# Optimization experiments

Measured on AMD Instinct MI355X. Metric: run time of the kernel, lower is better.

The kernel has to match this reference:

```python
import jax, jax.numpy as jnp
import numpy as np

N_QUBITS = 4
DIM = 2 ** N_QUBITS  # 16
B = 524288


def apply_1q(state, mat, wire):
    """Apply a 2x2 gate (mat: [2,2] or batched [B,2,2]) to `wire` of state [B,16]."""
    b = state.shape[0]
    s = state.reshape((b,) + (2,) * N_QUBITS)
    s = jnp.moveaxis(s, wire + 1, -1)
    shp = s.shape
    s = s.reshape(b, -1, 2)
    if mat.ndim == 3:
        s = jnp.einsum('bij,bkj->bki', mat, s)
    else:
        s = jnp.einsum('ij,bkj->bki', mat, s)
    s = jnp.moveaxis(s.reshape(shp), -1, wire + 1)
    return s.reshape(b, DIM)


def apply_2q(state, mat4, w1, w2):
    """Apply a 4x4 gate to wires (w1, w2) of state [B,16]; w1 is the high bit."""
    b = state.shape[0]
    s = state.reshape((b,) + (2,) * N_QUBITS)
    s = jnp.moveaxis(s, (w1 + 1, w2 + 1), (-2, -1))
    shp = s.shape
    s = s.reshape(b, -1, 4)
    s = jnp.einsum('ij,bkj->bki', mat4, s)
    s = jnp.moveaxis(s.reshape(shp), (-2, -1), (w1 + 1, w2 + 1))
    return s.reshape(b, DIM)


def rx_mat(t):
    c = jnp.cos(t / 2).astype(jnp.complex64)
    s = jnp.sin(t / 2).astype(jnp.complex64)
    return jnp.stack([jnp.stack([c, -1j * s]), jnp.stack([-1j * s, c])])


def ry_mat(t):
    c = jnp.cos(t / 2).astype(jnp.complex64)
    s = jnp.sin(t / 2).astype(jnp.complex64)
    return jnp.stack([jnp.stack([c, -s]), jnp.stack([s, c])])


def rz_mat(t):
    e0 = jnp.exp(-0.5j * t.astype(jnp.complex64))
    e1 = jnp.exp(0.5j * t.astype(jnp.complex64))
    z = jnp.zeros_like(e0)
    return jnp.stack([jnp.stack([e0, z]), jnp.stack([z, e1])])


CNOT = jnp.array([[1, 0, 0, 0],
                  [0, 1, 0, 0],
                  [0, 0, 0, 1],
                  [0, 0, 1, 0]], dtype=jnp.complex64)

# PauliZ sign table: sign of bit i (wire 0 = most significant axis) for each basis index
_idx = np.arange(DIM)
Z_SIGNS = jnp.asarray(
    1.0 - 2.0 * ((_idx[None, :] >> (N_QUBITS - 1 - np.arange(N_QUBITS)[:, None])) & 1),
    dtype=jnp.float32)  # [n_qubits, 16]


def setup_inputs() -> dict:
    key = jax.random.key(0)
    k1, k2 = jax.random.split(key)
    x = jax.random.normal(k1, (B, N_QUBITS), dtype=jnp.float32)
    params = jax.random.normal(k2, (6,), dtype=jnp.float32)
    return {"x": x, "params": params}


def reference(x, params):
    b = x.shape[0]
    state = jnp.zeros((b, DIM), jnp.complex64).at[:, 0].set(1.0)

    # --- RY encoding: angle x[:, i] on wire i (batched 2x2 matrices) ---
    for i in range(N_QUBITS):
        th = x[:, i]
        c = jnp.cos(th / 2).astype(jnp.complex64)
        s = jnp.sin(th / 2).astype(jnp.complex64)
        row0 = jnp.stack([c, -s], axis=-1)
        row1 = jnp.stack([s, c], axis=-1)
        mat = jnp.stack([row0, row1], axis=-2)  # [B,2,2]
        state = apply_1q(state, mat, i)

    # --- RandomLayer: fixed deterministic structure of 8 ops (6 rotations + 2 CNOTs) ---
    state = apply_1q(state, rx_mat(params[0]), 0)
    state = apply_1q(state, ry_mat(params[1]), 1)
    state = apply_1q(state, rz_mat(params[2]), 2)
    state = apply_1q(state, rx_mat(params[3]), 3)
    state = apply_2q(state, CNOT, 0, 1)
    state = apply_2q(state, CNOT, 2, 3)
    state = apply_1q(state, ry_mat(params[4]), 2)
    state = apply_1q(state, rz_mat(params[5]), 0)

    # --- MeasureAll(PauliZ): <Z_i> = sum_k |amp_k|^2 * sign(bit_i(k)) ---
    probs = state.real ** 2 + state.imag ** 2  # [B,16]
    return probs @ Z_SIGNS.T  # [B, n_qubits]
```

## Files before the change

kernel.cpp:

```cpp
#include <hip/hip_runtime.h>

struct cplx { float re, im; };

__device__ __forceinline__ cplx cmul(cplx a, cplx b) {
    return { a.re * b.re - a.im * b.im, a.re * b.im + a.im * b.re };
}
__device__ __forceinline__ cplx cadd(cplx a, cplx b) { return { a.re + b.re, a.im + b.im }; }

template<int MASK>
__device__ __forceinline__ void apply1(cplx st[16], cplx m00, cplx m01, cplx m10, cplx m11) {
#pragma unroll
    for (int i = 0; i < 16; ++i) {
        if (i & MASK) continue;
        cplx a0 = st[i], a1 = st[i | MASK];
        st[i]        = cadd(cmul(m00, a0), cmul(m01, a1));
        st[i | MASK] = cadd(cmul(m10, a0), cmul(m11, a1));
    }
}

__device__ __forceinline__ void cswap(cplx& a, cplx& b) { cplx t = a; a = b; b = t; }

__global__ __launch_bounds__(256) void qfilter_kernel(const float4* __restrict__ x,
                                                      const float* __restrict__ params,
                                                      float4* __restrict__ out, int B) {
    int b = blockIdx.x * blockDim.x + threadIdx.x;
    if (b >= B) return;

    float4 xv = x[b];
    float cx[4], sx[4];
    sincosf(0.5f * xv.x, &sx[0], &cx[0]);
    sincosf(0.5f * xv.y, &sx[1], &cx[1]);
    sincosf(0.5f * xv.z, &sx[2], &cx[2]);
    sincosf(0.5f * xv.w, &sx[3], &cx[3]);

    cplx st[16];
#pragma unroll
    for (int i = 0; i < 16; ++i) {
        float a = (((i >> 3) & 1) ? sx[0] : cx[0]) *
                  (((i >> 2) & 1) ? sx[1] : cx[1]) *
                  (((i >> 1) & 1) ? sx[2] : cx[2]) *
                  (((i     ) & 1) ? sx[3] : cx[3]);
        st[i] = { a, 0.0f };
    }

    float p0 = params[0], p1 = params[1], p2 = params[2], p3 = params[3], p4 = params[4];
    float c, s;

    sincosf(0.5f * p0, &s, &c);
    apply1<8>(st, {c, 0.f}, {0.f, -s}, {0.f, -s}, {c, 0.f});

    sincosf(0.5f * p1, &s, &c);
    apply1<4>(st, {c, 0.f}, {-s, 0.f}, {s, 0.f}, {c, 0.f});

    sincosf(0.5f * p2, &s, &c);
    apply1<2>(st, {c, -s}, {0.f, 0.f}, {0.f, 0.f}, {c, s});

    sincosf(0.5f * p3, &s, &c);
    apply1<1>(st, {c, 0.f}, {0.f, -s}, {0.f, -s}, {c, 0.f});

    cswap(st[8], st[12]); cswap(st[9], st[13]); cswap(st[10], st[14]); cswap(st[11], st[15]);

    cswap(st[2], st[3]); cswap(st[6], st[7]); cswap(st[10], st[11]); cswap(st[14], st[15]);

    sincosf(0.5f * p4, &s, &c);
    apply1<2>(st, {c, 0.f}, {-s, 0.f}, {s, 0.f}, {c, 0.f});


    float e0 = 0.f, e1 = 0.f, e2 = 0.f, e3 = 0.f;
#pragma unroll
    for (int i = 0; i < 16; ++i) {
        float pr = st[i].re * st[i].re + st[i].im * st[i].im;
        e0 += ((i >> 3) & 1) ? -pr : pr;
        e1 += ((i >> 2) & 1) ? -pr : pr;
        e2 += ((i >> 1) & 1) ? -pr : pr;
        e3 += ((i     ) & 1) ? -pr : pr;
    }
    out[b] = make_float4(e0, e1, e2, e3);
}

extern "C" void kernel_launch(void* const* d_in, const int* in_sizes, int n_in,
                              void* d_out, int out_size, void* d_ws, size_t ws_size,
                              hipStream_t stream) {
    const int B = in_sizes[0] / 4;
    const float4* x      = (const float4*)d_in[0];
    const float*  params = (const float*)d_in[1];
    float4*       out    = (float4*)d_out;

    const int threads = 256;
    const int blocks = (B + threads - 1) / threads;
    qfilter_kernel<<<blocks, threads, 0, stream>>>(x, params, out, B);
}
```

Before: 73.80 us.

## Replace statevector simulation with closed-form Pauli-Z expectation formulas

Derives analytic expressions for each qubit's <Z> expectation from the fixed circuit structure. This replaces the 16-amplitude complex statevector evolution with a few cosine and sine evaluations and products per sample. It also switches to fast intrinsics (__cosf/__sincosf), which trades accuracy for speed, and the derivation has to match the reference circuit exactly. The kernel is likely memory-bound, so the gain may come mostly from dropping instructions and registers.

```diff
diff --git a/kernel.cpp b/kernel.cpp
--- a/kernel.cpp
+++ b/kernel.cpp
@@ -1,24 +1,5 @@
 #include <hip/hip_runtime.h>
 
-struct cplx { float re, im; };
-
-__device__ __forceinline__ cplx cmul(cplx a, cplx b) {
-    return { a.re * b.re - a.im * b.im, a.re * b.im + a.im * b.re };
-}
-__device__ __forceinline__ cplx cadd(cplx a, cplx b) { return { a.re + b.re, a.im + b.im }; }
-
-template<int MASK>
-__device__ __forceinline__ void apply1(cplx st[16], cplx m00, cplx m01, cplx m10, cplx m11) {
-#pragma unroll
-    for (int i = 0; i < 16; ++i) {
-        if (i & MASK) continue;
-        cplx a0 = st[i], a1 = st[i | MASK];
-        st[i]        = cadd(cmul(m00, a0), cmul(m01, a1));
-        st[i | MASK] = cadd(cmul(m10, a0), cmul(m11, a1));
-    }
-}
-
-__device__ __forceinline__ void cswap(cplx& a, cplx& b) { cplx t = a; a = b; b = t; }
 
 __global__ __launch_bounds__(256) void qfilter_kernel(const float4* __restrict__ x,
                                                       const float* __restrict__ params,
@@ -27,55 +8,25 @@
     if (b >= B) return;
 
     float4 xv = x[b];
-    float cx[4], sx[4];
-    sincosf(0.5f * xv.x, &sx[0], &cx[0]);
-    sincosf(0.5f * xv.y, &sx[1], &cx[1]);
-    sincosf(0.5f * xv.z, &sx[2], &cx[2]);
-    sincosf(0.5f * xv.w, &sx[3], &cx[3]);
 
-    cplx st[16];
-#pragma unroll
-    for (int i = 0; i < 16; ++i) {
-        float a = (((i >> 3) & 1) ? sx[0] : cx[0]) *
-                  (((i >> 2) & 1) ? sx[1] : cx[1]) *
-                  (((i >> 1) & 1) ? sx[2] : cx[2]) *
-                  (((i     ) & 1) ? sx[3] : cx[3]);
-        st[i] = { a, 0.0f };
-    }
+    float p1  = params[1];
+    float cp0 = __cosf(params[0]);
+    float cp2 = __cosf(params[2]);
+    float cp3 = __cosf(params[3]);
+    float sp4, cp4;
+    __sincosf(params[4], &sp4, &cp4);
 
-    float p0 = params[0], p1 = params[1], p2 = params[2], p3 = params[3], p4 = params[4];
-    float c, s;
+    float c0 = __cosf(xv.x);
+    float c1 = __cosf(xv.y + p1);
+    float s2, c2; __sincosf(xv.z, &s2, &c2);
+    float s3, c3; __sincosf(xv.w, &s3, &c3);
 
-    sincosf(0.5f * p0, &s, &c);
-    apply1<8>(st, {c, 0.f}, {0.f, -s}, {0.f, -s}, {c, 0.f});
+    float o0 = cp0 * c0;
+    float o1 = o0 * c1;
+    float o2 = cp4 * c2 - sp4 * cp2 * s2 * s3;
+    float o3 = cp3 * c3 * c2;
 
-    sincosf(0.5f * p1, &s, &c);
-    apply1<4>(st, {c, 0.f}, {-s, 0.f}, {s, 0.f}, {c, 0.f});
-
-    sincosf(0.5f * p2, &s, &c);
-    apply1<2>(st, {c, -s}, {0.f, 0.f}, {0.f, 0.f}, {c, s});
-
-    sincosf(0.5f * p3, &s, &c);
-    apply1<1>(st, {c, 0.f}, {0.f, -s}, {0.f, -s}, {c, 0.f});
-
-    cswap(st[8], st[12]); cswap(st[9], st[13]); cswap(st[10], st[14]); cswap(st[11], st[15]);
-
-    cswap(st[2], st[3]); cswap(st[6], st[7]); cswap(st[10], st[11]); cswap(st[14], st[15]);
-
-    sincosf(0.5f * p4, &s, &c);
-    apply1<2>(st, {c, 0.f}, {-s, 0.f}, {s, 0.f}, {c, 0.f});
-
-
-    float e0 = 0.f, e1 = 0.f, e2 = 0.f, e3 = 0.f;
-#pragma unroll
-    for (int i = 0; i < 16; ++i) {
-        float pr = st[i].re * st[i].re + st[i].im * st[i].im;
-        e0 += ((i >> 3) & 1) ? -pr : pr;
-        e1 += ((i >> 2) & 1) ? -pr : pr;
-        e2 += ((i >> 1) & 1) ? -pr : pr;
-        e3 += ((i     ) & 1) ? -pr : pr;
-    }
-    out[b] = make_float4(e0, e1, e2, e3);
+    out[b] = make_float4(o0, o1, o2, o3);
 }
 
 extern "C" void kernel_launch(void* const* d_in, const int* in_sizes, int n_in,
```

Measured after the change: 60.71 us. 17.7% less time.
